# Optimization experiments

Hardware: AMD Instinct MI355X
Metric: run time of the kernel (lower is better)

Reference implementation:

```python
import jax, jax.numpy as jnp
import numpy as np

D_MODEL = 1024
H = 16
D_K = D_MODEL // H
B, S = 2, 2048
NEG = -1e9


def setup_inputs() -> dict:
    key = jax.random.key(0)
    ks = jax.random.split(key, 8)
    scale = 1.0 / np.sqrt(D_MODEL)
    q = jax.random.normal(ks[0], (B, S, D_MODEL), dtype=jnp.float32)
    k = jax.random.normal(ks[1], (B, S, D_MODEL), dtype=jnp.float32)
    v = jax.random.normal(ks[2], (B, S, D_MODEL), dtype=jnp.float32)
    # causal 0/1 mask, broadcastable to [B, h, S, S]
    mask = jnp.tril(jnp.ones((S, S), dtype=jnp.int32))[None, None, :, :]
    w_q = jax.random.normal(ks[3], (D_MODEL, D_MODEL), dtype=jnp.float32) * scale
    w_k = jax.random.normal(ks[4], (D_MODEL, D_MODEL), dtype=jnp.float32) * scale
    w_v = jax.random.normal(ks[5], (D_MODEL, D_MODEL), dtype=jnp.float32) * scale
    w_o = jax.random.normal(ks[6], (D_MODEL, D_MODEL), dtype=jnp.float32) * scale
    return {"q": q, "k": k, "v": v, "mask": mask,
            "w_q": w_q, "w_k": w_k, "w_v": w_v, "w_o": w_o}


def reference(q, k, v, mask, w_q, w_k, w_v, w_o):
    # projections (no bias)
    def split_heads(x):
        Bn, Sn, _ = x.shape
        return x.reshape(Bn, Sn, H, D_K).transpose(0, 2, 1, 3)  # [B,h,S,d_k]

    qh = split_heads(q @ w_q)
    kh = split_heads(k @ w_k)
    vh = split_heads(v @ w_v)

    scores = jnp.einsum('bhqd,bhkd->bhqk', qh, kh) / jnp.sqrt(
        jnp.asarray(D_K, dtype=qh.dtype))
    scores = jnp.where(mask == 0, jnp.asarray(NEG, dtype=scores.dtype), scores)
    attn = jax.nn.softmax(scores, axis=-1)  # dropout rate 0.0 -> identity
    x = jnp.einsum('bhqk,bhkd->bhqd', attn, vh)  # [B,h,S,d_k]
    x = x.transpose(0, 2, 1, 3).reshape(q.shape[0], q.shape[1], D_MODEL)
    return x @ w_o
```

## Files before the change

kernel.cpp:

```cpp
#include <hip/hip_runtime.h>

#define D_MODEL 1024
#define NH 16
#define DK 64
#define BB 2
#define SS 2048
#define M_TOT (BB*SS)

typedef float f32x4 __attribute__((ext_vector_type(4)));
typedef float f32x16 __attribute__((ext_vector_type(16)));
typedef __bf16 bf16x8 __attribute__((ext_vector_type(8)));
typedef unsigned int u32;

#define QSCALE 0.1803368801f
#define DEFER_THR 11.5416f

__device__ __forceinline__ unsigned short f2bf(float f){
  unsigned int u = __float_as_uint(f);
  unsigned int r = (u + 0x7fffu + ((u >> 16) & 1u)) >> 16;
  return (unsigned short)r;
}

__device__ __forceinline__ void gload_lds16(const void* g, void* l){
  __builtin_amdgcn_global_load_lds((const __attribute__((address_space(1))) void*)g,
                                   (__attribute__((address_space(3))) void*)l,
                                   16, 0, 0);
}

__device__ __forceinline__ void swap_half(u32 a, u32 b, int hi, u32& x, u32& y){
#if __has_builtin(__builtin_amdgcn_permlane32_swap)
  typedef unsigned int uint2v __attribute__((ext_vector_type(2)));
  uint2v r = __builtin_amdgcn_permlane32_swap(a, b, false, false);
  x = r.x; y = r.y;
#else
  u32 as = __shfl_xor(a, 32);
  u32 bs = __shfl_xor(b, 32);
  x = hi ? bs : a;
  y = hi ? b  : as;
#endif
}

__global__ __launch_bounds__(256) void transpose_cvt4(const float* __restrict__ wq,
                                                      const float* __restrict__ wk,
                                                      const float* __restrict__ wv,
                                                      const float* __restrict__ wo,
                                                      unsigned short* __restrict__ WqkvT,
                                                      unsigned short* __restrict__ woT){
  __shared__ float tile[64][65];
  const int which = blockIdx.z;
  const float* w = (which == 0) ? wq : (which == 1) ? wk : (which == 2) ? wv : wo;
  unsigned short* wt = (which == 3) ? woT : (WqkvT + (size_t)which * 1024 * 1024);
  const int N = D_MODEL;
  const int bx = blockIdx.x * 64;
  const int by = blockIdx.y * 64;
  const int t = threadIdx.x;
  #pragma unroll
  for (int i = 0; i < 16; ++i){
    int idx = t + i * 256;
    int r = idx >> 6, c = idx & 63;
    tile[r][c] = w[(size_t)(by + r) * N + bx + c];
  }
  __syncthreads();
  #pragma unroll
  for (int i = 0; i < 16; ++i){
    int idx = t + i * 256;
    int r = idx >> 6, c = idx & 63;
    wt[(size_t)(bx + r) * N + by + c] = f2bf(tile[c][r]);
  }
}

__global__ __launch_bounds__(256) void gemm_qkv(const float* __restrict__ Aq,
                                                const float* __restrict__ Ak,
                                                const float* __restrict__ Av,
                                                const unsigned short* __restrict__ WT,
                                                unsigned short* __restrict__ Qh,
                                                unsigned short* __restrict__ Kh,
                                                unsigned short* __restrict__ VhT){
  __shared__ unsigned short Al[2][128 * 32];
  __shared__ unsigned short Bl[2][128 * 32];
  const int tid = threadIdx.x;
  const int wid = tid >> 6, lane = tid & 63;
  const int lr = lane & 15, lg = lane >> 4;
  const int wm = wid >> 1, wn = wid & 1;
  const int bm = blockIdx.x, bn = blockIdx.y;
  const int seg = bn >> 3;
  const float* A = (seg == 0) ? Aq : (seg == 1) ? Ak : Av;
  const int K = D_MODEL;

  f32x4 acc[4][4];
  #pragma unroll
  for (int i = 0; i < 4; ++i)
    #pragma unroll
    for (int j = 0; j < 4; ++j)
      acc[i][j] = (f32x4){0.f, 0.f, 0.f, 0.f};

  const int arow  = tid >> 2;
  const int aslot = tid & 3;

  f32x4 ar[2][2];

  auto loadA = [&](int kt){
    #pragma unroll
    for (int p = 0; p < 2; ++p){
      const float* base = &A[(size_t)(bm * 128 + p * 64 + arow) * K + kt * 32 + aslot * 8];
      ar[p][0] = *(const f32x4*)(base);
      ar[p][1] = *(const f32x4*)(base + 4);
    }
  };
  auto writeA = [&](int buf){
    #pragma unroll
    for (int p = 0; p < 2; ++p){
      u32 cc[4];
      asm("v_cvt_pk_bf16_f32 %0, %1, %2" : "=v"(cc[0]) : "v"(ar[p][0][0]), "v"(ar[p][0][1]));
      asm("v_cvt_pk_bf16_f32 %0, %1, %2" : "=v"(cc[1]) : "v"(ar[p][0][2]), "v"(ar[p][0][3]));
      asm("v_cvt_pk_bf16_f32 %0, %1, %2" : "=v"(cc[2]) : "v"(ar[p][1][0]), "v"(ar[p][1][1]));
      asm("v_cvt_pk_bf16_f32 %0, %1, %2" : "=v"(cc[3]) : "v"(ar[p][1][2]), "v"(ar[p][1][3]));
      uint4 wv4 = {cc[0], cc[1], cc[2], cc[3]};
      *(uint4*)&Al[buf][(p * 64 + arow) * 32 + aslot * 8] = wv4;
    }
  };
  auto stageB = [&](int buf, int kt){
    #pragma unroll
    for (int rr = 0; rr < 2; ++rr){
      int vt = tid + rr * 256;
      int row = vt >> 2, c8 = (vt & 3) * 8;
      gload_lds16(WT + (size_t)(bn * 128 + row) * K + kt * 32 + c8,
                  &Bl[buf][(wid << 9) + rr * 2048]);
    }
  };

  loadA(0);
  stageB(0, 0);
  writeA(0);

  int cur = 0;
  for (int kt = 0; kt < 32; ++kt){
    __syncthreads();
    if (kt + 1 < 32){
      loadA(kt + 1);
      stageB(cur ^ 1, kt + 1);
    }
    bf16x8 af[4], bfr[4];
    #pragma unroll
    for (int i = 0; i < 4; ++i)
      af[i] = *(const bf16x8*)&Al[cur][(wm * 64 + i * 16 + lr) * 32 + lg * 8];
    #pragma unroll
    for (int j = 0; j < 4; ++j)
      bfr[j] = *(const bf16x8*)&Bl[cur][(wn * 64 + j * 16 + lr) * 32 + lg * 8];
    #pragma unroll
    for (int i = 0; i < 4; ++i)
      #pragma unroll
      for (int j = 0; j < 4; ++j)
        acc[i][j] = __builtin_amdgcn_mfma_f32_16x16x32_bf16(af[i], bfr[j], acc[i][j], 0, 0, 0);
    if (kt + 1 < 32) writeA(cur ^ 1);
    cur ^= 1;
  }

  if (seg < 2){
    unsigned short* O = (seg == 0) ? Qh : Kh;
    const float sc = (seg == 0) ? QSCALE : 1.0f;
    #pragma unroll
    for (int i = 0; i < 4; ++i){
      int row0 = bm * 128 + wm * 64 + i * 16 + lg * 4;
      #pragma unroll
      for (int j = 0; j < 4; ++j){
        int colseg = (bn & 7) * 128 + wn * 64 + j * 16 + lr;
        int h = colseg >> 6, dk = colseg & 63;
        #pragma unroll
        for (int p = 0; p < 4; ++p){
          int rowm = row0 + p;
          int b = rowm >> 11, s = rowm & 2047;
          O[((size_t)(b * NH + h) * SS + s) * DK + dk] = f2bf(acc[i][j][p] * sc);
        }
      }
    }
  } else {
    #pragma unroll
    for (int i = 0; i < 4; ++i){
      int row0 = bm * 128 + wm * 64 + i * 16 + lg * 4;
      int b = row0 >> 11, s = row0 & 2047;
      #pragma unroll
      for (int j = 0; j < 4; ++j){
        int colseg = (bn & 7) * 128 + wn * 64 + j * 16 + lr;
        int h = colseg >> 6, dk = colseg & 63;
        ushort4 o4;
        o4.x = f2bf(acc[i][j][0]); o4.y = f2bf(acc[i][j][1]);
        o4.z = f2bf(acc[i][j][2]); o4.w = f2bf(acc[i][j][3]);
        *(ushort4*)&VhT[((size_t)(b * NH + h) * DK + dk) * SS + s] = o4;
      }
    }
  }
}

__global__ __launch_bounds__(256) void gemm_o64(const unsigned short* __restrict__ A,
                                                const unsigned short* __restrict__ Bt,
                                                float* __restrict__ O){
  __shared__ unsigned short Al[2][64 * 32];
  __shared__ unsigned short Bl[2][128 * 32];
  const int tid = threadIdx.x;
  const int wid = tid >> 6, lane = tid & 63;
  const int lr = lane & 15, lg = lane >> 4;
  const int wm = wid >> 1, wn = wid & 1;
  const int bm = blockIdx.x, bn = blockIdx.y;
  const int K = D_MODEL;

  f32x4 acc[2][4];
  #pragma unroll
  for (int i = 0; i < 2; ++i)
    #pragma unroll
    for (int j = 0; j < 4; ++j)
      acc[i][j] = (f32x4){0.f, 0.f, 0.f, 0.f};

  auto stage = [&](int buf, int kt){
    {
      int row = tid >> 2, c8 = (tid & 3) * 8;
      gload_lds16(A + (size_t)(bm * 64 + row) * K + kt * 32 + c8,
                  &Al[buf][wid << 9]);
    }
    #pragma unroll
    for (int r = 0; r < 2; ++r){
      int vt = tid + r * 256;
      int row = vt >> 2, c8 = (vt & 3) * 8;
      gload_lds16(Bt + (size_t)(bn * 128 + row) * K + kt * 32 + c8,
                  &Bl[buf][(wid << 9) + r * 2048]);
    }
  };

  stage(0, 0);
  int cur = 0;
  for (int kt = 0; kt < 32; ++kt){
    __syncthreads();
    if (kt + 1 < 32) stage(cur ^ 1, kt + 1);
    bf16x8 af[2], bfr[4];
    #pragma unroll
    for (int i = 0; i < 2; ++i)
      af[i] = *(const bf16x8*)&Al[cur][(wm * 32 + i * 16 + lr) * 32 + lg * 8];
    #pragma unroll
    for (int j = 0; j < 4; ++j)
      bfr[j] = *(const bf16x8*)&Bl[cur][(wn * 64 + j * 16 + lr) * 32 + lg * 8];
    #pragma unroll
    for (int i = 0; i < 2; ++i)
      #pragma unroll
      for (int j = 0; j < 4; ++j)
        acc[i][j] = __builtin_amdgcn_mfma_f32_16x16x32_bf16(af[i], bfr[j], acc[i][j], 0, 0, 0);
    cur ^= 1;
  }

  #pragma unroll
  for (int i = 0; i < 2; ++i){
    int row0 = bm * 64 + wm * 32 + i * 16 + lg * 4;
    #pragma unroll
    for (int j = 0; j < 4; ++j){
      int col = bn * 128 + wn * 64 + j * 16 + lr;
      #pragma unroll
      for (int p = 0; p < 4; ++p)
        O[(size_t)(row0 + p) * D_MODEL + col] = acc[i][j][p];
    }
  }
}

__global__ __launch_bounds__(256) void attn_kernel(const unsigned short* __restrict__ Qh,
                                                   const unsigned short* __restrict__ Kh,
                                                   const unsigned short* __restrict__ VhT,
                                                   unsigned short* __restrict__ Oc){
  __shared__ unsigned short SL[2][4][4096];
  const int bh = blockIdx.x;
  const int px = blockIdx.y;
  const int tid = threadIdx.x, wid = tid >> 6, lane = tid & 63;
  const int ln = lane & 31, hi = lane >> 5;
  const int qh = wid & 1, pp = wid >> 1;
  const int b = bh >> 4, h = bh & 15;
  const size_t kvbase = (size_t)bh * SS * DK;

  #pragma unroll 1
  for (int segq = 0; segq < 2; ++segq){
    const int qblk = segq ? (31 - px) : px;
    const int q0 = qblk * 64 + qh * 32;
    const int Tw = 2 * qblk + qh;
    const int R = (qblk + 2) >> 1;

    const unsigned short* qp = Qh + kvbase + (size_t)(q0 + ln) * DK + hi * 8;
    bf16x8 qbv[4];
    #pragma unroll
    for (int c = 0; c < 4; ++c) qbv[c] = *(const bf16x8*)(qp + c * 16);

    f32x16 oa0 = {0,0,0,0,0,0,0,0,0,0,0,0,0,0,0,0};
    f32x16 oa1 = {0,0,0,0,0,0,0,0,0,0,0,0,0,0,0,0};
    float m = -1e30f, ls = 0.f;

    auto stage = [&](int bufb, int r){
      const int k0A = (2 * r) * 64;
      const int k0B = k0A + 64;
      const bool haveB = (2 * r + 1) <= qblk;
      #pragma unroll
      for (int i = 0; i < 2; ++i){
        const int c = i * 256 + tid;
        const int row = c >> 3;
        const int slot = (c & 7) ^ (row & 7);
        const int ldso = (i * 256 + wid * 64) * 8;
        gload_lds16(Kh  + kvbase + (size_t)(k0A + row) * DK + slot * 8, &SL[bufb][0][ldso]);
        gload_lds16(VhT + kvbase + (size_t)row * SS + k0A + slot * 8,   &SL[bufb][1][ldso]);
        if (haveB){
          gload_lds16(Kh  + kvbase + (size_t)(k0B + row) * DK + slot * 8, &SL[bufb][2][ldso]);
          gload_lds16(VhT + kvbase + (size_t)row * SS + k0B + slot * 8,   &SL[bufb][3][ldso]);
        }
      }
    };

    stage(0, 0);
    int cur = 0;
    #pragma unroll 1
    for (int r = 0; r < R; ++r){
      __syncthreads();
      if (r + 1 < R) stage(cur ^ 1, r + 1);

      const int t = 2 * r + pp;
      if (t <= qblk){
        const unsigned short* Kb = SL[cur][pp * 2];
        const unsigned short* Vb = SL[cur][pp * 2 + 1];

        f32x16 sta = {0,0,0,0,0,0,0,0,0,0,0,0,0,0,0,0};
        f32x16 stb = {0,0,0,0,0,0,0,0,0,0,0,0,0,0,0,0};
        __builtin_amdgcn_s_setprio(1);
        #pragma unroll
        for (int c = 0; c < 4; ++c){
          const int po = ((c * 2 + hi) ^ (ln & 7)) * 8;
          bf16x8 kfa = *(const bf16x8*)&Kb[ln * 64 + po];
          bf16x8 kfb = *(const bf16x8*)&Kb[(32 + ln) * 64 + po];
          sta = __builtin_amdgcn_mfma_f32_32x32x16_bf16(kfa, qbv[c], sta, 0, 0, 0);
          stb = __builtin_amdgcn_mfma_f32_32x32x16_bf16(kfb, qbv[c], stb, 0, 0, 0);
        }
        __builtin_amdgcn_s_setprio(0);

        const int ta = 2 * t, tb = 2 * t + 1;
        if (tb == Tw){
          #pragma unroll
          for (int rr = 0; rr < 16; ++rr){
            int kg = (rr & 3) + 8 * (rr >> 2) + 4 * hi;
            if (kg > ln) stb[rr] = -1e30f;
          }
        } else if (ta == Tw){
          #pragma unroll
          for (int rr = 0; rr < 16; ++rr){
            int kg = (rr & 3) + 8 * (rr >> 2) + 4 * hi;
            if (kg > ln) sta[rr] = -1e30f;
            stb[rr] = -1e30f;
          }
        }

        float tm[8];
        #pragma unroll
        for (int i = 0; i < 8; ++i)
          tm[i] = fmaxf(fmaxf(sta[2*i], sta[2*i+1]), fmaxf(stb[2*i], stb[2*i+1]));
        float mx = fmaxf(fmaxf(fmaxf(tm[0], tm[1]), fmaxf(tm[2], tm[3])),
                         fmaxf(fmaxf(tm[4], tm[5]), fmaxf(tm[6], tm[7])));
        mx = fmaxf(mx, __shfl_xor(mx, 32));

        if (__any(mx > m + DEFER_THR)){
          const float mn = fmaxf(m, mx);
          const float fac = __builtin_amdgcn_exp2f(m - mn);
          m = mn;
          ls *= fac;
          #pragma unroll
          for (int rr = 0; rr < 16; ++rr){ oa0[rr] *= fac; oa1[rr] *= fac; }
        }

        #pragma unroll
        for (int rr = 0; rr < 16; ++rr){
          sta[rr] = __builtin_amdgcn_exp2f(sta[rr] - m);
          stb[rr] = __builtin_amdgcn_exp2f(stb[rr] - m);
        }
        float sm[8];
        #pragma unroll
        for (int i = 0; i < 8; ++i)
          sm[i] = (sta[2*i] + sta[2*i+1]) + (stb[2*i] + stb[2*i+1]);
        float rsum = ((sm[0] + sm[1]) + (sm[2] + sm[3])) + ((sm[4] + sm[5]) + (sm[6] + sm[7]));
        rsum += __shfl_xor(rsum, 32);
        ls += rsum;

        u32 ca[8], cb[8];
        #pragma unroll
        for (int i = 0; i < 8; ++i){
          asm("v_cvt_pk_bf16_f32 %0, %1, %2" : "=v"(ca[i]) : "v"(sta[2*i]), "v"(sta[2*i+1]));
          asm("v_cvt_pk_bf16_f32 %0, %1, %2" : "=v"(cb[i]) : "v"(stb[2*i]), "v"(stb[2*i+1]));
        }
        u32 w0[4], w1[4], w2[4], w3[4];
        swap_half(ca[0], ca[2], hi, w0[0], w0[2]);
        swap_half(ca[1], ca[3], hi, w0[1], w0[3]);
        swap_half(ca[4], ca[6], hi, w1[0], w1[2]);
        swap_half(ca[5], ca[7], hi, w1[1], w1[3]);
        swap_half(cb[0], cb[2], hi, w2[0], w2[2]);
        swap_half(cb[1], cb[3], hi, w2[1], w2[3]);
        swap_half(cb[4], cb[6], hi, w3[0], w3[2]);
        swap_half(cb[5], cb[7], hi, w3[1], w3[3]);
        bf16x8 pf[4];
        __builtin_memcpy(&pf[0], w0, 16);
        __builtin_memcpy(&pf[1], w1, 16);
        __builtin_memcpy(&pf[2], w2, 16);
        __builtin_memcpy(&pf[3], w3, 16);

        __builtin_amdgcn_s_setprio(1);
        #pragma unroll
        for (int ks = 0; ks < 4; ++ks){
          const int po = ((ks * 2 + hi) ^ (ln & 7)) * 8;
          bf16x8 v0 = *(const bf16x8*)&Vb[ln * 64 + po];
          bf16x8 v1 = *(const bf16x8*)&Vb[(32 + ln) * 64 + po];
          oa0 = __builtin_amdgcn_mfma_f32_32x32x16_bf16(v0, pf[ks], oa0, 0, 0, 0);
          oa1 = __builtin_amdgcn_mfma_f32_32x32x16_bf16(v1, pf[ks], oa1, 0, 0, 0);
        }
        __builtin_amdgcn_s_setprio(0);
      }
      cur ^= 1;
    }
    __syncthreads();

    float* oL  = (float*)&SL[0][0][0];
    float* mLs = (float*)&SL[0][2][0];
    if (wid >= 2){
      const int w = wid - 2;
      #pragma unroll
      for (int rr = 0; rr < 16; ++rr){
        oL[(w * 32 + rr) * 64 + lane]      = oa0[rr];
        oL[(w * 32 + 16 + rr) * 64 + lane] = oa1[rr];
      }
      if (hi == 0){ mLs[w * 32 + ln] = m; mLs[64 + w * 32 + ln] = ls; }
    }
    __syncthreads();
    if (wid < 2){
      const float m1  = mLs[wid * 32 + ln];
      const float ls1 = mLs[64 + wid * 32 + ln];
      const float mstar = fmaxf(m, m1);
      const float f0 = __builtin_amdgcn_exp2f(m  - mstar);
      const float f1 = __builtin_amdgcn_exp2f(m1 - mstar);
      const float inv = 1.0f / (f0 * ls + f1 * ls1);
      const size_t rowbase = ((size_t)b * SS + q0 + ln) * D_MODEL + h * DK;
      #pragma unroll
      for (int g = 0; g < 4; ++g){
        ushort4 o4;
        o4.x = f2bf((f0 * oa0[4*g + 0] + f1 * oL[(wid * 32 + 4*g + 0) * 64 + lane]) * inv);
        o4.y = f2bf((f0 * oa0[4*g + 1] + f1 * oL[(wid * 32 + 4*g + 1) * 64 + lane]) * inv);
        o4.z = f2bf((f0 * oa0[4*g + 2] + f1 * oL[(wid * 32 + 4*g + 2) * 64 + lane]) * inv);
        o4.w = f2bf((f0 * oa0[4*g + 3] + f1 * oL[(wid * 32 + 4*g + 3) * 64 + lane]) * inv);
        *(ushort4*)&Oc[rowbase + 8*g + 4*hi] = o4;
      }
      #pragma unroll
      for (int g = 0; g < 4; ++g){
        ushort4 o4;
        o4.x = f2bf((f0 * oa1[4*g + 0] + f1 * oL[(wid * 32 + 16 + 4*g + 0) * 64 + lane]) * inv);
        o4.y = f2bf((f0 * oa1[4*g + 1] + f1 * oL[(wid * 32 + 16 + 4*g + 1) * 64 + lane]) * inv);
        o4.z = f2bf((f0 * oa1[4*g + 2] + f1 * oL[(wid * 32 + 16 + 4*g + 2) * 64 + lane]) * inv);
        o4.w = f2bf((f0 * oa1[4*g + 3] + f1 * oL[(wid * 32 + 16 + 4*g + 3) * 64 + lane]) * inv);
        *(ushort4*)&Oc[rowbase + 32 + 8*g + 4*hi] = o4;
      }
    }
    __syncthreads();
  }
}

extern "C" void kernel_launch(void* const* d_in, const int* in_sizes, int n_in,
                              void* d_out, int out_size, void* d_ws, size_t ws_size,
                              hipStream_t stream){
  const float* q  = (const float*)d_in[0];
  const float* k  = (const float*)d_in[1];
  const float* v  = (const float*)d_in[2];
  const float* wq = (const float*)d_in[4];
  const float* wk = (const float*)d_in[5];
  const float* wv = (const float*)d_in[6];
  const float* wo = (const float*)d_in[7];
  float* out = (float*)d_out;

  char* ws = (char*)d_ws;
  const size_t MB = 1024 * 1024;
  unsigned short* WqkvT  = (unsigned short*)(ws + 0 * MB);
  unsigned short* woT    = (unsigned short*)(ws + 6 * MB);
  unsigned short* Qh     = (unsigned short*)(ws + 8 * MB);
  unsigned short* Kh     = (unsigned short*)(ws + 16 * MB);
  unsigned short* VhT    = (unsigned short*)(ws + 24 * MB);
  unsigned short* attnb  = (unsigned short*)(ws + 32 * MB);

  dim3 tg(16, 16, 4);
  transpose_cvt4<<<tg, 256, 0, stream>>>(wq, wk, wv, wo, WqkvT, woT);

  dim3 gqkv(M_TOT / 128, 3 * D_MODEL / 128);
  gemm_qkv<<<gqkv, 256, 0, stream>>>(q, k, v, WqkvT, Qh, Kh, VhT);

  dim3 ga(BB * NH, SS / 128);
  attn_kernel<<<ga, 256, 0, stream>>>(Qh, Kh, VhT, attnb);

  dim3 go(M_TOT / 64, D_MODEL / 128);
  gemm_o64<<<go, 256, 0, stream>>>(attnb, woT, out);
}
```

Baseline: 114.2 us.

## Process 128-row query blocks per workgroup, reusing K/V tiles across two query tiles

The attention kernel now gives each wave two 32-row query tiles instead of one, so every K/V fragment read from LDS feeds twice as many MFMAs. The old two-segment paired loop is replaced by a single pass over a 128-query block, with blockIdx.y mapped so short and long causal rows interleave across the grid. The grid keeps 16 blocks in y, but each block now covers 128 queries. This raises register pressure (four output accumulators and eight score tiles per wave) and may leave the causal load less balanced across blocks.

```diff
diff --git a/kernel.cpp b/kernel.cpp
--- a/kernel.cpp
+++ b/kernel.cpp
@@ -264,196 +264,220 @@
                                                    const unsigned short* __restrict__ VhT,
                                                    unsigned short* __restrict__ Oc){
   __shared__ unsigned short SL[2][4][4096];
+  __shared__ float mlsL[2][2][2][32];
   const int bh = blockIdx.x;
-  const int px = blockIdx.y;
+  const int y = blockIdx.y;
+  const int P = (y < 8) ? y : (23 - y);
   const int tid = threadIdx.x, wid = tid >> 6, lane = tid & 63;
   const int ln = lane & 31, hi = lane >> 5;
   const int qh = wid & 1, pp = wid >> 1;
   const int b = bh >> 4, h = bh & 15;
   const size_t kvbase = (size_t)bh * SS * DK;
-
+  const int qt0 = 4 * P + 2 * qh;
+  const int qt1 = qt0 + 1;
+  const int R = P + 1;
+
+  bf16x8 qv0[4], qv1[4];
+  {
+    const unsigned short* qp0 = Qh + kvbase + (size_t)(32 * qt0 + ln) * DK + hi * 8;
+    const unsigned short* qp1 = Qh + kvbase + (size_t)(32 * qt1 + ln) * DK + hi * 8;
+    #pragma unroll
+    for (int c = 0; c < 4; ++c){
+      qv0[c] = *(const bf16x8*)(qp0 + c * 16);
+      qv1[c] = *(const bf16x8*)(qp1 + c * 16);
+    }
+  }
+
+  f32x16 oaA0 = {0,0,0,0,0,0,0,0,0,0,0,0,0,0,0,0};
+  f32x16 oaB0 = {0,0,0,0,0,0,0,0,0,0,0,0,0,0,0,0};
+  f32x16 oaA1 = {0,0,0,0,0,0,0,0,0,0,0,0,0,0,0,0};
+  f32x16 oaB1 = {0,0,0,0,0,0,0,0,0,0,0,0,0,0,0,0};
+  float m0 = -1e30f, ls0 = 0.f, m1 = -1e30f, ls1 = 0.f;
+
+  auto stage = [&](int bufb, int r){
+    const int k0A = (2 * r) * 64;
+    const int k0B = k0A + 64;
+    #pragma unroll
+    for (int i = 0; i < 2; ++i){
+      const int c = i * 256 + tid;
+      const int row = c >> 3;
+      const int slot = (c & 7) ^ (row & 7);
+      const int ldso = (i * 256 + wid * 64) * 8;
+      gload_lds16(Kh  + kvbase + (size_t)(k0A + row) * DK + slot * 8, &SL[bufb][0][ldso]);
+      gload_lds16(VhT + kvbase + (size_t)row * SS + k0A + slot * 8,   &SL[bufb][1][ldso]);
+      gload_lds16(Kh  + kvbase + (size_t)(k0B + row) * DK + slot * 8, &SL[bufb][2][ldso]);
+      gload_lds16(VhT + kvbase + (size_t)row * SS + k0B + slot * 8,   &SL[bufb][3][ldso]);
+    }
+  };
+
+  auto softmax1 = [&](f32x16& sta, f32x16& stb, float& m, float& ls,
+                      f32x16& oaA, f32x16& oaB, bf16x8 (&pf)[4]){
+    float tm[8];
+    #pragma unroll
+    for (int i = 0; i < 8; ++i)
+      tm[i] = fmaxf(fmaxf(sta[2*i], sta[2*i+1]), fmaxf(stb[2*i], stb[2*i+1]));
+    float mx = fmaxf(fmaxf(fmaxf(tm[0], tm[1]), fmaxf(tm[2], tm[3])),
+                     fmaxf(fmaxf(tm[4], tm[5]), fmaxf(tm[6], tm[7])));
+    mx = fmaxf(mx, __shfl_xor(mx, 32));
+    if (__any(mx > m + DEFER_THR)){
+      const float mn = fmaxf(m, mx);
+      const float fac = __builtin_amdgcn_exp2f(m - mn);
+      m = mn;
+      ls *= fac;
+      #pragma unroll
+      for (int rr = 0; rr < 16; ++rr){ oaA[rr] *= fac; oaB[rr] *= fac; }
+    }
+    #pragma unroll
+    for (int rr = 0; rr < 16; ++rr){
+      sta[rr] = __builtin_amdgcn_exp2f(sta[rr] - m);
+      stb[rr] = __builtin_amdgcn_exp2f(stb[rr] - m);
+    }
+    float sm[8];
+    #pragma unroll
+    for (int i = 0; i < 8; ++i)
+      sm[i] = (sta[2*i] + sta[2*i+1]) + (stb[2*i] + stb[2*i+1]);
+    float rsum = ((sm[0] + sm[1]) + (sm[2] + sm[3])) + ((sm[4] + sm[5]) + (sm[6] + sm[7]));
+    rsum += __shfl_xor(rsum, 32);
+    ls += rsum;
+    u32 ca[8], cb[8];
+    #pragma unroll
+    for (int i = 0; i < 8; ++i){
+      asm("v_cvt_pk_bf16_f32 %0, %1, %2" : "=v"(ca[i]) : "v"(sta[2*i]), "v"(sta[2*i+1]));
+      asm("v_cvt_pk_bf16_f32 %0, %1, %2" : "=v"(cb[i]) : "v"(stb[2*i]), "v"(stb[2*i+1]));
+    }
+    u32 w0[4], w1[4], w2[4], w3[4];
+    swap_half(ca[0], ca[2], hi, w0[0], w0[2]);
+    swap_half(ca[1], ca[3], hi, w0[1], w0[3]);
+    swap_half(ca[4], ca[6], hi, w1[0], w1[2]);
+    swap_half(ca[5], ca[7], hi, w1[1], w1[3]);
+    swap_half(cb[0], cb[2], hi, w2[0], w2[2]);
+    swap_half(cb[1], cb[3], hi, w2[1], w2[3]);
+    swap_half(cb[4], cb[6], hi, w3[0], w3[2]);
+    swap_half(cb[5], cb[7], hi, w3[1], w3[3]);
+    __builtin_memcpy(&pf[0], w0, 16);
+    __builtin_memcpy(&pf[1], w1, 16);
+    __builtin_memcpy(&pf[2], w2, 16);
+    __builtin_memcpy(&pf[3], w3, 16);
+  };
+
+  stage(0, 0);
+  int cur = 0;
   #pragma unroll 1
-  for (int segq = 0; segq < 2; ++segq){
-    const int qblk = segq ? (31 - px) : px;
-    const int q0 = qblk * 64 + qh * 32;
-    const int Tw = 2 * qblk + qh;
-    const int R = (qblk + 2) >> 1;
-
-    const unsigned short* qp = Qh + kvbase + (size_t)(q0 + ln) * DK + hi * 8;
-    bf16x8 qbv[4];
-    #pragma unroll
-    for (int c = 0; c < 4; ++c) qbv[c] = *(const bf16x8*)(qp + c * 16);
-
-    f32x16 oa0 = {0,0,0,0,0,0,0,0,0,0,0,0,0,0,0,0};
-    f32x16 oa1 = {0,0,0,0,0,0,0,0,0,0,0,0,0,0,0,0};
-    float m = -1e30f, ls = 0.f;
-
-    auto stage = [&](int bufb, int r){
-      const int k0A = (2 * r) * 64;
-      const int k0B = k0A + 64;
-      const bool haveB = (2 * r + 1) <= qblk;
-      #pragma unroll
-      for (int i = 0; i < 2; ++i){
-        const int c = i * 256 + tid;
-        const int row = c >> 3;
-        const int slot = (c & 7) ^ (row & 7);
-        const int ldso = (i * 256 + wid * 64) * 8;
-        gload_lds16(Kh  + kvbase + (size_t)(k0A + row) * DK + slot * 8, &SL[bufb][0][ldso]);
-        gload_lds16(VhT + kvbase + (size_t)row * SS + k0A + slot * 8,   &SL[bufb][1][ldso]);
-        if (haveB){
-          gload_lds16(Kh  + kvbase + (size_t)(k0B + row) * DK + slot * 8, &SL[bufb][2][ldso]);
-          gload_lds16(VhT + kvbase + (size_t)row * SS + k0B + slot * 8,   &SL[bufb][3][ldso]);
-        }
-      }
-    };
-
-    stage(0, 0);
-    int cur = 0;
-    #pragma unroll 1
-    for (int r = 0; r < R; ++r){
-      __syncthreads();
-      if (r + 1 < R) stage(cur ^ 1, r + 1);
-
-      const int t = 2 * r + pp;
-      if (t <= qblk){
-        const unsigned short* Kb = SL[cur][pp * 2];
-        const unsigned short* Vb = SL[cur][pp * 2 + 1];
-
-        f32x16 sta = {0,0,0,0,0,0,0,0,0,0,0,0,0,0,0,0};
-        f32x16 stb = {0,0,0,0,0,0,0,0,0,0,0,0,0,0,0,0};
-        __builtin_amdgcn_s_setprio(1);
-        #pragma unroll
-        for (int c = 0; c < 4; ++c){
-          const int po = ((c * 2 + hi) ^ (ln & 7)) * 8;
-          bf16x8 kfa = *(const bf16x8*)&Kb[ln * 64 + po];
-          bf16x8 kfb = *(const bf16x8*)&Kb[(32 + ln) * 64 + po];
-          sta = __builtin_amdgcn_mfma_f32_32x32x16_bf16(kfa, qbv[c], sta, 0, 0, 0);
-          stb = __builtin_amdgcn_mfma_f32_32x32x16_bf16(kfb, qbv[c], stb, 0, 0, 0);
-        }
-        __builtin_amdgcn_s_setprio(0);
-
-        const int ta = 2 * t, tb = 2 * t + 1;
-        if (tb == Tw){
-          #pragma unroll
-          for (int rr = 0; rr < 16; ++rr){
-            int kg = (rr & 3) + 8 * (rr >> 2) + 4 * hi;
-            if (kg > ln) stb[rr] = -1e30f;
-          }
-        } else if (ta == Tw){
-          #pragma unroll
-          for (int rr = 0; rr < 16; ++rr){
-            int kg = (rr & 3) + 8 * (rr >> 2) + 4 * hi;
-            if (kg > ln) sta[rr] = -1e30f;
-            stb[rr] = -1e30f;
-          }
-        }
-
-        float tm[8];
-        #pragma unroll
-        for (int i = 0; i < 8; ++i)
-          tm[i] = fmaxf(fmaxf(sta[2*i], sta[2*i+1]), fmaxf(stb[2*i], stb[2*i+1]));
-        float mx = fmaxf(fmaxf(fmaxf(tm[0], tm[1]), fmaxf(tm[2], tm[3])),
-                         fmaxf(fmaxf(tm[4], tm[5]), fmaxf(tm[6], tm[7])));
-        mx = fmaxf(mx, __shfl_xor(mx, 32));
-
-        if (__any(mx > m + DEFER_THR)){
-          const float mn = fmaxf(m, mx);
-          const float fac = __builtin_amdgcn_exp2f(m - mn);
-          m = mn;
-          ls *= fac;
-          #pragma unroll
-          for (int rr = 0; rr < 16; ++rr){ oa0[rr] *= fac; oa1[rr] *= fac; }
-        }
-
+  for (int r = 0; r < R; ++r){
+    __syncthreads();
+    if (r + 1 < R) stage(cur ^ 1, r + 1);
+
+    const int t = 2 * r + pp;
+    const bool act = (2 * t <= qt0);
+    if (act){
+      const unsigned short* Kb = SL[cur][pp * 2];
+      const unsigned short* Vb = SL[cur][pp * 2 + 1];
+
+      f32x16 sta0 = {0,0,0,0,0,0,0,0,0,0,0,0,0,0,0,0};
+      f32x16 stb0 = {0,0,0,0,0,0,0,0,0,0,0,0,0,0,0,0};
+      f32x16 sta1 = {0,0,0,0,0,0,0,0,0,0,0,0,0,0,0,0};
+      f32x16 stb1 = {0,0,0,0,0,0,0,0,0,0,0,0,0,0,0,0};
+      __builtin_amdgcn_s_setprio(1);
+      #pragma unroll
+      for (int c = 0; c < 4; ++c){
+        const int po = ((c * 2 + hi) ^ (ln & 7)) * 8;
+        bf16x8 kfa = *(const bf16x8*)&Kb[ln * 64 + po];
+        bf16x8 kfb = *(const bf16x8*)&Kb[(32 + ln) * 64 + po];
+        sta0 = __builtin_amdgcn_mfma_f32_32x32x16_bf16(kfa, qv0[c], sta0, 0, 0, 0);
+        stb0 = __builtin_amdgcn_mfma_f32_32x32x16_bf16(kfb, qv0[c], stb0, 0, 0, 0);
+        sta1 = __builtin_amdgcn_mfma_f32_32x32x16_bf16(kfa, qv1[c], sta1, 0, 0, 0);
+        stb1 = __builtin_amdgcn_mfma_f32_32x32x16_bf16(kfb, qv1[c], stb1, 0, 0, 0);
+      }
+      __builtin_amdgcn_s_setprio(0);
+
+      const int ta = 2 * t, tb = 2 * t + 1;
+      if (ta == qt0){
         #pragma unroll
         for (int rr = 0; rr < 16; ++rr){
-          sta[rr] = __builtin_amdgcn_exp2f(sta[rr] - m);
-          stb[rr] = __builtin_amdgcn_exp2f(stb[rr] - m);
+          int kg = (rr & 3) + 8 * (rr >> 2) + 4 * hi;
+          if (kg > ln) sta0[rr] = -1e30f;
+          stb0[rr] = -1e30f;
         }
-        float sm[8];
+      }
+      if (tb == qt1){
         #pragma unroll
-        for (int i = 0; i < 8; ++i)
-          sm[i] = (sta[2*i] + sta[2*i+1]) + (stb[2*i] + stb[2*i+1]);
-        float rsum = ((sm[0] + sm[1]) + (sm[2] + sm[3])) + ((sm[4] + sm[5]) + (sm[6] + sm[7]));
-        rsum += __shfl_xor(rsum, 32);
-        ls += rsum;
-
-        u32 ca[8], cb[8];
-        #pragma unroll
-        for (int i = 0; i < 8; ++i){
-          asm("v_cvt_pk_bf16_f32 %0, %1, %2" : "=v"(ca[i]) : "v"(sta[2*i]), "v"(sta[2*i+1]));
-          asm("v_cvt_pk_bf16_f32 %0, %1, %2" : "=v"(cb[i]) : "v"(stb[2*i]), "v"(stb[2*i+1]));
+        for (int rr = 0; rr < 16; ++rr){
+          int kg = (rr & 3) + 8 * (rr >> 2) + 4 * hi;
+          if (kg > ln) stb1[rr] = -1e30f;
         }
-        u32 w0[4], w1[4], w2[4], w3[4];
-        swap_half(ca[0], ca[2], hi, w0[0], w0[2]);
-        swap_half(ca[1], ca[3], hi, w0[1], w0[3]);
-        swap_half(ca[4], ca[6], hi, w1[0], w1[2]);
-        swap_half(ca[5], ca[7], hi, w1[1], w1[3]);
-        swap_half(cb[0], cb[2], hi, w2[0], w2[2]);
-        swap_half(cb[1], cb[3], hi, w2[1], w2[3]);
-        swap_half(cb[4], cb[6], hi, w3[0], w3[2]);
-        swap_half(cb[5], cb[7], hi, w3[1], w3[3]);
-        bf16x8 pf[4];
-        __builtin_memcpy(&pf[0], w0, 16);
-        __builtin_memcpy(&pf[1], w1, 16);
-        __builtin_memcpy(&pf[2], w2, 16);
-        __builtin_memcpy(&pf[3], w3, 16);
-
-        __builtin_amdgcn_s_setprio(1);
-        #pragma unroll
-        for (int ks = 0; ks < 4; ++ks){
-          const int po = ((ks * 2 + hi) ^ (ln & 7)) * 8;
-          bf16x8 v0 = *(const bf16x8*)&Vb[ln * 64 + po];
-          bf16x8 v1 = *(const bf16x8*)&Vb[(32 + ln) * 64 + po];
-          oa0 = __builtin_amdgcn_mfma_f32_32x32x16_bf16(v0, pf[ks], oa0, 0, 0, 0);
-          oa1 = __builtin_amdgcn_mfma_f32_32x32x16_bf16(v1, pf[ks], oa1, 0, 0, 0);
-        }
-        __builtin_amdgcn_s_setprio(0);
-      }
-      cur ^= 1;
-    }
-    __syncthreads();
-
-    float* oL  = (float*)&SL[0][0][0];
-    float* mLs = (float*)&SL[0][2][0];
-    if (wid >= 2){
-      const int w = wid - 2;
-      #pragma unroll
-      for (int rr = 0; rr < 16; ++rr){
-        oL[(w * 32 + rr) * 64 + lane]      = oa0[rr];
-        oL[(w * 32 + 16 + rr) * 64 + lane] = oa1[rr];
-      }
-      if (hi == 0){ mLs[w * 32 + ln] = m; mLs[64 + w * 32 + ln] = ls; }
-    }
-    __syncthreads();
-    if (wid < 2){
-      const float m1  = mLs[wid * 32 + ln];
-      const float ls1 = mLs[64 + wid * 32 + ln];
-      const float mstar = fmaxf(m, m1);
-      const float f0 = __builtin_amdgcn_exp2f(m  - mstar);
-      const float f1 = __builtin_amdgcn_exp2f(m1 - mstar);
-      const float inv = 1.0f / (f0 * ls + f1 * ls1);
-      const size_t rowbase = ((size_t)b * SS + q0 + ln) * D_MODEL + h * DK;
+      }
+
+      bf16x8 pf0[4], pf1[4];
+      softmax1(sta0, stb0, m0, ls0, oaA0, oaB0, pf0);
+      softmax1(sta1, stb1, m1, ls1, oaA1, oaB1, pf1);
+
+      __builtin_amdgcn_s_setprio(1);
+      #pragma unroll
+      for (int ks = 0; ks < 4; ++ks){
+        const int po = ((ks * 2 + hi) ^ (ln & 7)) * 8;
+        bf16x8 v0 = *(const bf16x8*)&Vb[ln * 64 + po];
+        bf16x8 v1 = *(const bf16x8*)&Vb[(32 + ln) * 64 + po];
+        oaA0 = __builtin_amdgcn_mfma_f32_32x32x16_bf16(v0, pf0[ks], oaA0, 0, 0, 0);
+        oaB0 = __builtin_amdgcn_mfma_f32_32x32x16_bf16(v1, pf0[ks], oaB0, 0, 0, 0);
+        oaA1 = __builtin_amdgcn_mfma_f32_32x32x16_bf16(v0, pf1[ks], oaA1, 0, 0, 0);
+        oaB1 = __builtin_amdgcn_mfma_f32_32x32x16_bf16(v1, pf1[ks], oaB1, 0, 0, 0);
+      }
+      __builtin_amdgcn_s_setprio(0);
+    }
+    cur ^= 1;
+  }
+  __syncthreads();
+
+  float* oL = (float*)&SL[0][0][0];
+  if (pp == 1){
+    #pragma unroll
+    for (int rr = 0; rr < 16; ++rr){
+      oL[((qh * 2 + 0) * 32 + rr)      * 64 + lane] = oaA0[rr];
+      oL[((qh * 2 + 0) * 32 + 16 + rr) * 64 + lane] = oaB0[rr];
+      oL[((qh * 2 + 1) * 32 + rr)      * 64 + lane] = oaA1[rr];
+      oL[((qh * 2 + 1) * 32 + 16 + rr) * 64 + lane] = oaB1[rr];
+    }
+    if (hi == 0){
+      mlsL[qh][0][0][ln] = m0; mlsL[qh][0][1][ln] = ls0;
+      mlsL[qh][1][0][ln] = m1; mlsL[qh][1][1][ln] = ls1;
+    }
+  }
+  __syncthreads();
+  if (pp == 0){
+    #pragma unroll
+    for (int j = 0; j < 2; ++j){
+      const float mj  = (j == 0) ? m0  : m1;
+      const float lsj = (j == 0) ? ls0 : ls1;
+      const f32x16& oaAj = (j == 0) ? oaA0 : oaA1;
+      const f32x16& oaBj = (j == 0) ? oaB0 : oaB1;
+      const float mp  = mlsL[qh][j][0][ln];
+      const float lsp = mlsL[qh][j][1][ln];
+      const float mstar = fmaxf(mj, mp);
+      const float f0 = __builtin_amdgcn_exp2f(mj - mstar);
+      const float f1 = __builtin_amdgcn_exp2f(mp - mstar);
+      const float inv = 1.0f / (f0 * lsj + f1 * lsp);
+      const int qt = qt0 + j;
+      const float* oLj = &oL[(qh * 2 + j) * 32 * 64];
+      const size_t rowbase = ((size_t)b * SS + 32 * qt + ln) * D_MODEL + h * DK;
       #pragma unroll
       for (int g = 0; g < 4; ++g){
         ushort4 o4;
-        o4.x = f2bf((f0 * oa0[4*g + 0] + f1 * oL[(wid * 32 + 4*g + 0) * 64 + lane]) * inv);
-        o4.y = f2bf((f0 * oa0[4*g + 1] + f1 * oL[(wid * 32 + 4*g + 1) * 64 + lane]) * inv);
-        o4.z = f2bf((f0 * oa0[4*g + 2] + f1 * oL[(wid * 32 + 4*g + 2) * 64 + lane]) * inv);
-        o4.w = f2bf((f0 * oa0[4*g + 3] + f1 * oL[(wid * 32 + 4*g + 3) * 64 + lane]) * inv);
+        o4.x = f2bf((f0 * oaAj[4*g + 0] + f1 * oLj[(4*g + 0) * 64 + lane]) * inv);
+        o4.y = f2bf((f0 * oaAj[4*g + 1] + f1 * oLj[(4*g + 1) * 64 + lane]) * inv);
+        o4.z = f2bf((f0 * oaAj[4*g + 2] + f1 * oLj[(4*g + 2) * 64 + lane]) * inv);
+        o4.w = f2bf((f0 * oaAj[4*g + 3] + f1 * oLj[(4*g + 3) * 64 + lane]) * inv);
         *(ushort4*)&Oc[rowbase + 8*g + 4*hi] = o4;
       }
       #pragma unroll
       for (int g = 0; g < 4; ++g){
         ushort4 o4;
-        o4.x = f2bf((f0 * oa1[4*g + 0] + f1 * oL[(wid * 32 + 16 + 4*g + 0) * 64 + lane]) * inv);
-        o4.y = f2bf((f0 * oa1[4*g + 1] + f1 * oL[(wid * 32 + 16 + 4*g + 1) * 64 + lane]) * inv);
-        o4.z = f2bf((f0 * oa1[4*g + 2] + f1 * oL[(wid * 32 + 16 + 4*g + 2) * 64 + lane]) * inv);
-        o4.w = f2bf((f0 * oa1[4*g + 3] + f1 * oL[(wid * 32 + 16 + 4*g + 3) * 64 + lane]) * inv);
+        o4.x = f2bf((f0 * oaBj[4*g + 0] + f1 * oLj[(16 + 4*g + 0) * 64 + lane]) * inv);
+        o4.y = f2bf((f0 * oaBj[4*g + 1] + f1 * oLj[(16 + 4*g + 1) * 64 + lane]) * inv);
+        o4.z = f2bf((f0 * oaBj[4*g + 2] + f1 * oLj[(16 + 4*g + 2) * 64 + lane]) * inv);
+        o4.w = f2bf((f0 * oaBj[4*g + 3] + f1 * oLj[(16 + 4*g + 3) * 64 + lane]) * inv);
         *(ushort4*)&Oc[rowbase + 32 + 8*g + 4*hi] = o4;
       }
     }
-    __syncthreads();
   }
 }
 
@@ -484,7 +508,7 @@
   dim3 gqkv(M_TOT / 128, 3 * D_MODEL / 128);
   gemm_qkv<<<gqkv, 256, 0, stream>>>(q, k, v, WqkvT, Qh, Kh, VhT);
 
-  dim3 ga(BB * NH, SS / 128);
+  dim3 ga(BB * NH, 16);
   attn_kernel<<<ga, 256, 0, stream>>>(Qh, Kh, VhT, attnb);
 
   dim3 go(M_TOT / 64, D_MODEL / 128);
```

After: 120.4 us. 5.5% more time.
